# Kernel tuning notes

Measured on AMD Instinct MI355X. Metric: run time of the kernel, lower is better.

Reference implementation:

```python
import jax, jax.numpy as jnp
import numpy as np
import math

B, C, L_MIX, L_REF = 4, 512, 2048, 2048
NUM_HEADS = 8
HEAD_DIM = C // NUM_HEADS
MAX_LEN = 5000
EPS = 1e-5


def layer_norm(x, gamma, beta):
    mu = jnp.mean(x, axis=-1, keepdims=True)
    var = jnp.mean(jnp.square(x - mu), axis=-1, keepdims=True)
    return (x - mu) * jax.lax.rsqrt(var + EPS) * gamma + beta


def setup_inputs() -> dict:
    key = jax.random.key(0)
    ks = jax.random.split(key, 12)
    inp = {
        "query": jax.random.normal(ks[0], (B, C, L_MIX), dtype=jnp.float32),
        "key_value": jax.random.normal(ks[1], (B, C, L_REF), dtype=jnp.float32),
        "pos_encoding": jax.random.normal(ks[2], (1, MAX_LEN, C), dtype=jnp.float32) * 0.01,
        "q_gamma": jnp.ones((C,), jnp.float32),
        "q_beta": jnp.zeros((C,), jnp.float32),
        "k_gamma": jnp.ones((C,), jnp.float32),
        "k_beta": jnp.zeros((C,), jnp.float32),
        "Wq": jax.random.normal(ks[3], (C, C), jnp.float32) / math.sqrt(C),
        "bq": jax.random.normal(ks[4], (C,), jnp.float32) * 0.01,
        "Wk": jax.random.normal(ks[5], (C, C), jnp.float32) / math.sqrt(C),
        "bk": jax.random.normal(ks[6], (C,), jnp.float32) * 0.01,
        "Wv": jax.random.normal(ks[7], (C, C), jnp.float32) / math.sqrt(C),
        "bv": jax.random.normal(ks[8], (C,), jnp.float32) * 0.01,
        "Wo": jax.random.normal(ks[9], (C, C), jnp.float32) / math.sqrt(C),
        "bo": jax.random.normal(ks[10], (C,), jnp.float32) * 0.01,
    }
    return inp


def reference(query, key_value, pos_encoding, q_gamma, q_beta, k_gamma, k_beta,
              Wq, bq, Wk, bk, Wv, bv, Wo, bo):
    # (B, C, L) -> (B, L, C)
    q = jnp.transpose(query, (0, 2, 1))
    kv = jnp.transpose(key_value, (0, 2, 1))
    Lm, Lr = q.shape[1], kv.shape[1]
    q = q + pos_encoding[:, :Lm, :]
    kv = kv + pos_encoding[:, :Lr, :]
    q = layer_norm(q, q_gamma, q_beta)
    kv = layer_norm(kv, k_gamma, k_beta)
    Q = q @ Wq + bq          # (B, Lm, C)
    K = kv @ Wk + bk         # (B, Lr, C)
    V = kv @ Wv + bv         # (B, Lr, C)
    Q = Q.reshape(B, Lm, NUM_HEADS, HEAD_DIM)
    K = K.reshape(B, Lr, NUM_HEADS, HEAD_DIM)
    V = V.reshape(B, Lr, NUM_HEADS, HEAD_DIM)
    scale = math.sqrt(HEAD_DIM)
    scores = jnp.einsum('bqhd,bkhd->bhqk', Q, K) / scale  # (B, H, Lm, Lr)
    scores = jnp.clip(scores, -50.0, 50.0)
    attn = jax.nn.softmax(scores, axis=-1)  # dropout is identity at eval
    out = jnp.einsum('bhqk,bkhd->bqhd', attn, V).reshape(B, Lm, C)
    out = out @ Wo + bo
    out = out + q            # residual with normed/pos-encoded query, per source
    return jnp.transpose(out, (0, 2, 1))  # (B, C, Lm)
```

## Files before the change

### kernel.cpp

```cpp
#include <hip/hip_runtime.h>
#include <hip/hip_bf16.h>

#define B_ 4
#define C_ 512
#define L_ 2048
#define H_ 8
#define D_ 64
#define EPS_ 1e-5f

using short8 = __attribute__((ext_vector_type(8))) short;
using s4v    = __attribute__((ext_vector_type(4))) short;
using f32x4  = __attribute__((ext_vector_type(4))) float;

#if defined(__has_builtin)
#if __has_builtin(__builtin_amdgcn_exp2f)
#define EXP2(x) __builtin_amdgcn_exp2f(x)
#else
#define EXP2(x) exp2f(x)
#endif
#else
#define EXP2(x) exp2f(x)
#endif

#define GLOAD_LDS16(g, l)                                                     \
  __builtin_amdgcn_global_load_lds(                                           \
      (const __attribute__((address_space(1))) void*)(g),                     \
      (__attribute__((address_space(3))) void*)(l), 16, 0, 0)

static __device__ __forceinline__ short f2bf(float f) {
  __hip_bfloat16 h = __float2bfloat16(f);
  return __builtin_bit_cast(short, h);
}
static __device__ __forceinline__ float bf2f(short s) {
  return __bfloat162float(__builtin_bit_cast(__hip_bfloat16, s));
}

__global__ __launch_bounds__(256) void k_convert_w(
    const float* __restrict__ Wq, const float* __restrict__ Wk,
    const float* __restrict__ Wv, const float* __restrict__ Wo,
    short* __restrict__ Wt) {
  int m = blockIdx.x, k0 = blockIdx.y * 32, n0 = blockIdx.z * 32;
  const float* W = (m == 0) ? Wq : (m == 1) ? Wk : (m == 2) ? Wv : Wo;
  __shared__ float T[32][33];
  int t = threadIdx.x;
  {
    int kl = t >> 3, n4 = (t & 7) * 4;
    float4 v = *(const float4*)(W + (size_t)(k0 + kl) * C_ + n0 + n4);
    T[kl][n4] = v.x; T[kl][n4 + 1] = v.y; T[kl][n4 + 2] = v.z; T[kl][n4 + 3] = v.w;
  }
  __syncthreads();
  {
    int nl = t >> 3, k4 = (t & 7) * 4;
    s4v o;
#pragma unroll
    for (int j = 0; j < 4; ++j) o[j] = f2bf(T[k4 + j][nl]);
    *(s4v*)(Wt + (size_t)(m * C_ + n0 + nl) * C_ + k0 + k4) = o;
  }
}

__global__ __launch_bounds__(256) void k_prep(
    const float* __restrict__ query, const float* __restrict__ kv,
    const float* __restrict__ pos,
    const float* __restrict__ qg, const float* __restrict__ qb,
    const float* __restrict__ kg, const float* __restrict__ kb,
    short* __restrict__ qn, short* __restrict__ kvn) {
  int l0 = blockIdx.x * 16;
  int b  = blockIdx.y;
  int z  = blockIdx.z;
  const float* src = z ? kv : query;
  const float* g   = z ? kg : qg;
  const float* be  = z ? kb : qb;
  short* dst       = z ? kvn : qn;

  __shared__ alignas(16) float T[16][516];
  __shared__ float mu_s[16], rs_s[16];
  int t = threadIdx.x;

#pragma unroll
  for (int i = 0; i < 8; ++i) {
    int idx = i * 256 + t;
    int cc = idx >> 2, lg = (idx & 3) * 4;
    float4 v = *(const float4*)(src + (size_t)(b * C_ + cc) * L_ + l0 + lg);
    T[lg + 0][cc] = v.x; T[lg + 1][cc] = v.y; T[lg + 2][cc] = v.z; T[lg + 3][cc] = v.w;
  }
  __syncthreads();
#pragma unroll
  for (int i = 0; i < 8; ++i) {
    int idx = i * 256 + t;
    int ll = idx >> 7, c4 = (idx & 127) * 4;
    float4 p = *(const float4*)(pos + (size_t)(l0 + ll) * C_ + c4);
    float4* tp = (float4*)&T[ll][c4];
    float4 cur = *tp;
    cur.x += p.x; cur.y += p.y; cur.z += p.z; cur.w += p.w;
    *tp = cur;
  }
  __syncthreads();
  {
    int row = t >> 4, j = t & 15;
    float s1 = 0.f, s2 = 0.f;
    for (int c = j; c < C_; c += 16) { float v = T[row][c]; s1 += v; s2 += v * v; }
    for (int m = 1; m < 16; m <<= 1) {
      s1 += __shfl_xor(s1, m, 64);
      s2 += __shfl_xor(s2, m, 64);
    }
    if (j == 0) {
      float mu  = s1 * (1.0f / C_);
      float var = s2 * (1.0f / C_) - mu * mu;
      mu_s[row] = mu;
      rs_s[row] = rsqrtf(var + EPS_);
    }
  }
  __syncthreads();
#pragma unroll
  for (int i = 0; i < 8; ++i) {
    int idx = i * 256 + t;
    int ll = idx >> 7, c4 = (idx & 127) * 4;
    float4 v  = *(const float4*)&T[ll][c4];
    float4 gv = *(const float4*)(g + c4);
    float4 bv = *(const float4*)(be + c4);
    float mu = mu_s[ll], rs = rs_s[ll];
    s4v o;
    o[0] = f2bf((v.x - mu) * rs * gv.x + bv.x);
    o[1] = f2bf((v.y - mu) * rs * gv.y + bv.y);
    o[2] = f2bf((v.z - mu) * rs * gv.z + bv.z);
    o[3] = f2bf((v.w - mu) * rs * gv.w + bv.w);
    *(s4v*)(dst + (size_t)(b * L_ + l0 + ll) * C_ + c4) = o;
  }
}

__global__ __launch_bounds__(256) void k_gemm_qkv(
    const short* __restrict__ qn, const short* __restrict__ kvn,
    const short* __restrict__ Wt,
    const float* __restrict__ bq, const float* __restrict__ bk, const float* __restrict__ bv,
    short* __restrict__ Qw, short* __restrict__ Kw, short* __restrict__ Vtg) {
  int z = blockIdx.z;
  const short* X    = z ? kvn : qn;
  const short* W    = Wt + (size_t)z * C_ * C_;
  const float* bias = (z == 0) ? bq : (z == 1) ? bk : bv;
  float sc          = (z == 0) ? 0.18033688f : 1.0f;

  int m0 = blockIdx.x * 128, n0 = blockIdx.y * 128;
  __shared__ alignas(16) short As[128 * 32];
  __shared__ alignas(16) short Bs[128 * 32];
  int t = threadIdx.x, lane = t & 63, w = t >> 6;
  int wm = w & 1, wn = w >> 1;
  int quad = lane >> 4, c = lane & 15;

  const short* Ag = X + (size_t)(m0 + w * 32 + (lane >> 2)) * C_ + (lane & 3) * 8;
  const short* Bg = W + (size_t)(n0 + w * 32 + (lane >> 2)) * C_ + (lane & 3) * 8;

  f32x4 zero4 = {0.f, 0.f, 0.f, 0.f};
  f32x4 acc[4][4];
  for (int i = 0; i < 4; ++i) for (int j = 0; j < 4; ++j) acc[i][j] = zero4;

  for (int k0 = 0; k0 < C_; k0 += 32) {
    __syncthreads();
#pragma unroll
    for (int j = 0; j < 2; ++j) {
      GLOAD_LDS16(Ag + (size_t)j * 16 * C_ + k0, As + (w * 32 + j * 16) * 32);
      GLOAD_LDS16(Bg + (size_t)j * 16 * C_ + k0, Bs + (w * 32 + j * 16) * 32);
    }
    __syncthreads();
    short8 a[4], bf[4];
#pragma unroll
    for (int i = 0; i < 4; ++i)
      a[i]  = *(const short8*)(As + (wm * 64 + i * 16 + c) * 32 + quad * 8);
#pragma unroll
    for (int i = 0; i < 4; ++i)
      bf[i] = *(const short8*)(Bs + (wn * 64 + i * 16 + c) * 32 + quad * 8);
#pragma unroll
    for (int i = 0; i < 4; ++i)
#pragma unroll
      for (int j = 0; j < 4; ++j)
        acc[i][j] = __builtin_amdgcn_mfma_f32_16x16x32_bf16(a[i], bf[j], acc[i][j], 0, 0, 0);
  }

  if (z == 2) {
#pragma unroll
    for (int i = 0; i < 4; ++i)
#pragma unroll
      for (int j = 0; j < 4; ++j) {
        int colg = n0 + wn * 64 + j * 16 + c;
        float bia = bias[colg];
        int hh = colg >> 6, dd = colg & 63;
        int rowg = m0 + wm * 64 + i * 16 + quad * 4;
        int bb = rowg >> 11, l = rowg & (L_ - 1);
        s4v o;
#pragma unroll
        for (int r = 0; r < 4; ++r) o[r] = f2bf(acc[i][j][r] + bia);
        *(s4v*)(Vtg + ((size_t)(bb * H_ + hh) * D_ + dd) * L_ + l) = o;
      }
  } else {
    short* Y = (z == 0) ? Qw : Kw;
#pragma unroll
    for (int i = 0; i < 4; ++i)
#pragma unroll
      for (int j = 0; j < 4; ++j) {
        int colg = n0 + wn * 64 + j * 16 + c;
        float bia = bias[colg];
        int rowg = m0 + wm * 64 + i * 16 + quad * 4;
#pragma unroll
        for (int r = 0; r < 4; ++r)
          Y[(size_t)(rowg + r) * C_ + colg] = f2bf((acc[i][j][r] + bia) * sc);
      }
  }
}

#define LDP 72
#define LDC 68
__global__ __launch_bounds__(256, 2) void k_attn(
    const short* __restrict__ Qw, const short* __restrict__ Kw,
    const short* __restrict__ Vtg, short* __restrict__ Ow) {
  int bh = blockIdx.x & 31;
  int l0 = (blockIdx.x >> 5) * 128;
  int b = bh >> 3, h = bh & 7;
  __shared__ alignas(16) short Pw[4][16 * LDP];
  __shared__ alignas(16) float Cbuf[128 * LDC];
  __shared__ float Lbuf[128];
  int t = threadIdx.x, lane = t & 63, w = t >> 6;
  int qh = w & 1, ls = w >> 1;
  int quad = lane >> 4, c = lane & 15;

  short8 qa[4][2];
#pragma unroll
  for (int s = 0; s < 4; ++s) {
    const short* qp = Qw + ((size_t)(b * L_ + l0 + qh * 64 + s * 16 + c) * H_ + h) * D_ + quad * 8;
    qa[s][0] = *(const short8*)qp;
    qa[s][1] = *(const short8*)(qp + 32);
  }

  f32x4 zero4 = {0.f, 0.f, 0.f, 0.f};
  f32x4 acc[4][4];
#pragma unroll
  for (int s = 0; s < 4; ++s)
    for (int dt = 0; dt < 4; ++dt) acc[s][dt] = zero4;
  float lsum[4] = {0.f, 0.f, 0.f, 0.f};

  const short* Kb = Kw + ((size_t)(b * L_) * H_ + h) * D_;
  const short* Vb = Vtg + (size_t)(b * H_ + h) * D_ * L_;
  short* pb = &Pw[w][0];

  short8 kf[2][4][2];
  auto loadK = [&](int buf, int lr) {
#pragma unroll
    for (int T = 0; T < 4; ++T) {
      const short* kp = Kb + (size_t)(lr + T * 16 + c) * C_ + quad * 8;
      kf[buf][T][0] = *(const short8*)kp;
      kf[buf][T][1] = *(const short8*)(kp + 32);
    }
  };

  auto chunk = [&](int buf, int lr0, int lrn) {
    loadK(buf ^ 1, lrn);
    short8 vf[4][2];
#pragma unroll
    for (int dt = 0; dt < 4; ++dt) {
      const short* vp = Vb + (size_t)(dt * 16 + c) * L_ + lr0 + quad * 8;
      vf[dt][0] = *(const short8*)vp;
      vf[dt][1] = *(const short8*)(vp + 32);
    }
#pragma unroll
    for (int s = 0; s < 4; ++s) {
      f32x4 st[4] = {zero4, zero4, zero4, zero4};
#pragma unroll
      for (int T = 0; T < 4; ++T) {
        st[T] = __builtin_amdgcn_mfma_f32_16x16x32_bf16(kf[buf][T][0], qa[s][0], st[T], 0, 0, 0);
        st[T] = __builtin_amdgcn_mfma_f32_16x16x32_bf16(kf[buf][T][1], qa[s][1], st[T], 0, 0, 0);
      }
#pragma unroll
      for (int T = 0; T < 4; ++T) {
        s4v pk;
#pragma unroll
        for (int r = 0; r < 4; ++r) {
          float p = EXP2(st[T][r]);
          lsum[s] += p;
          pk[r] = f2bf(p);
        }
        *(s4v*)(pb + c * LDP + T * 16 + quad * 4) = pk;
      }
#pragma unroll
      for (int hf = 0; hf < 2; ++hf) {
        short8 pf = *(const short8*)(pb + c * LDP + hf * 32 + quad * 8);
#pragma unroll
        for (int dt = 0; dt < 4; ++dt)
          acc[s][dt] = __builtin_amdgcn_mfma_f32_16x16x32_bf16(vf[dt][hf], pf, acc[s][dt], 0, 0, 0);
      }
    }
  };

  loadK(0, ls * 64);
  for (int i = 0; i < 8; ++i) {
    int lr0 = ls * 64 + i * 256;
    chunk(0, lr0, lr0 + 128);
    chunk(1, lr0 + 128, (i == 7) ? ls * 64 : lr0 + 256);
  }

#pragma unroll
  for (int s = 0; s < 4; ++s) {
    lsum[s] += __shfl_xor(lsum[s], 16, 64);
    lsum[s] += __shfl_xor(lsum[s], 32, 64);
  }

  if (ls == 1) {
#pragma unroll
    for (int s = 0; s < 4; ++s) {
      int q = qh * 64 + s * 16 + c;
#pragma unroll
      for (int dt = 0; dt < 4; ++dt)
        *(f32x4*)(Cbuf + q * LDC + dt * 16 + quad * 4) = acc[s][dt];
      if (quad == 0) Lbuf[q] = lsum[s];
    }
  }
  __syncthreads();
  if (ls == 0) {
#pragma unroll
    for (int s = 0; s < 4; ++s) {
      int q = qh * 64 + s * 16 + c;
      float inv = 1.0f / (lsum[s] + Lbuf[q]);
#pragma unroll
      for (int dt = 0; dt < 4; ++dt) {
        f32x4 o = *(const f32x4*)(Cbuf + q * LDC + dt * 16 + quad * 4);
        s4v ov;
#pragma unroll
        for (int r = 0; r < 4; ++r) ov[r] = f2bf((acc[s][dt][r] + o[r]) * inv);
        *(s4v*)(Ow + ((size_t)(b * L_ + l0 + q) * H_ + h) * D_ + dt * 16 + quad * 4) = ov;
      }
    }
  }
}

__global__ __launch_bounds__(256) void k_gemm_out(
    const short* __restrict__ Ow, const short* __restrict__ Wot,
    const float* __restrict__ bo, const short* __restrict__ qn,
    float* __restrict__ out) {
  int m0 = blockIdx.x * 128, n0 = blockIdx.y * 128;
  __shared__ alignas(16) short As[128 * 32];
  __shared__ alignas(16) short Bs[128 * 32];
  int t = threadIdx.x, lane = t & 63, w = t >> 6;
  int wm = w & 1, wn = w >> 1;
  int quad = lane >> 4, c = lane & 15;

  const short* Ag = Ow  + (size_t)(m0 + w * 32 + (lane >> 2)) * C_ + (lane & 3) * 8;
  const short* Bg = Wot + (size_t)(n0 + w * 32 + (lane >> 2)) * C_ + (lane & 3) * 8;

  f32x4 zero4 = {0.f, 0.f, 0.f, 0.f};
  f32x4 acc[4][4];
  for (int i = 0; i < 4; ++i) for (int j = 0; j < 4; ++j) acc[i][j] = zero4;

  for (int k0 = 0; k0 < C_; k0 += 32) {
    __syncthreads();
#pragma unroll
    for (int j = 0; j < 2; ++j) {
      GLOAD_LDS16(Ag + (size_t)j * 16 * C_ + k0, As + (w * 32 + j * 16) * 32);
      GLOAD_LDS16(Bg + (size_t)j * 16 * C_ + k0, Bs + (w * 32 + j * 16) * 32);
    }
    __syncthreads();
    short8 a[4], bf[4];
#pragma unroll
    for (int i = 0; i < 4; ++i)
      a[i]  = *(const short8*)(As + (wm * 64 + i * 16 + c) * 32 + quad * 8);
#pragma unroll
    for (int i = 0; i < 4; ++i)
      bf[i] = *(const short8*)(Bs + (wn * 64 + i * 16 + c) * 32 + quad * 8);
#pragma unroll
    for (int i = 0; i < 4; ++i)
#pragma unroll
      for (int j = 0; j < 4; ++j)
        acc[i][j] = __builtin_amdgcn_mfma_f32_16x16x32_bf16(a[i], bf[j], acc[i][j], 0, 0, 0);
  }

  int bb = m0 >> 11;
#pragma unroll
  for (int i = 0; i < 4; ++i)
#pragma unroll
    for (int j = 0; j < 4; ++j) {
      int colg = n0 + wn * 64 + j * 16 + c;
      float bia = bo[colg];
      int rowg = m0 + wm * 64 + i * 16 + quad * 4;
      int l = rowg & (L_ - 1);
      float4 vv;
      float* pv = &vv.x;
#pragma unroll
      for (int r = 0; r < 4; ++r)
        pv[r] = acc[i][j][r] + bia + bf2f(qn[(size_t)(rowg + r) * C_ + colg]);
      *(float4*)(out + ((size_t)bb * C_ + colg) * L_ + l) = vv;
    }
}

extern "C" void kernel_launch(void* const* d_in, const int* in_sizes, int n_in,
                              void* d_out, int out_size, void* d_ws, size_t ws_size,
                              hipStream_t stream) {
  const float* query     = (const float*)d_in[0];
  const float* key_value = (const float*)d_in[1];
  const float* pos       = (const float*)d_in[2];
  const float* qg        = (const float*)d_in[3];
  const float* qb        = (const float*)d_in[4];
  const float* kg        = (const float*)d_in[5];
  const float* kb        = (const float*)d_in[6];
  const float* Wq        = (const float*)d_in[7];
  const float* bq        = (const float*)d_in[8];
  const float* Wk        = (const float*)d_in[9];
  const float* bk        = (const float*)d_in[10];
  const float* Wv        = (const float*)d_in[11];
  const float* bv        = (const float*)d_in[12];
  const float* Wo        = (const float*)d_in[13];
  const float* bo        = (const float*)d_in[14];
  float* out = (float*)d_out;

  char* ws = (char*)d_ws;
  const size_t SZ = (size_t)B_ * L_ * C_ * 2;
  short* qn  = (short*)(ws + 0 * SZ);
  short* kvn = (short*)(ws + 1 * SZ);
  short* Qw  = (short*)(ws + 2 * SZ);
  short* Kw  = (short*)(ws + 3 * SZ);
  short* Vtg = (short*)(ws + 4 * SZ);
  short* Ow  = (short*)(ws + 5 * SZ);
  short* Wt  = (short*)(ws + 6 * SZ);

  k_convert_w<<<dim3(4, 16, 16), 256, 0, stream>>>(Wq, Wk, Wv, Wo, Wt);
  k_prep<<<dim3(L_ / 16, B_, 2), 256, 0, stream>>>(query, key_value, pos, qg, qb, kg, kb, qn, kvn);
  k_gemm_qkv<<<dim3(8192 / 128, C_ / 128, 3), 256, 0, stream>>>(qn, kvn, Wt, bq, bk, bv, Qw, Kw, Vtg);
  k_attn<<<dim3(512), 256, 0, stream>>>(Qw, Kw, Vtg, Ow);
  k_gemm_out<<<dim3(8192 / 128, C_ / 128, 1), 256, 0, stream>>>(Ow, Wt + (size_t)3 * C_ * C_, bo, qn, out);
}
```

Baseline: 280.1 us.

## Merge weight-convert and prep kernels, widen GEMM K-tile, simplify attention loop

Fuses the weight transpose/convert kernel and the layernorm prep kernel into one launch, with block-index dispatch over a shared LDS buffer. This removes one kernel launch. Both projection GEMMs now stage 64-wide K tiles instead of 32, which halves the number of barrier pairs per tile at the cost of double the LDS. The attention loop drops the register double-buffered K prefetch in favour of a simpler per-chunk load of K and V. That lowers register pressure but exposes load latency.

```diff
diff --git a/kernel.cpp b/kernel.cpp
--- a/kernel.cpp
+++ b/kernel.cpp
@@ -35,46 +35,52 @@
   return __bfloat162float(__builtin_bit_cast(__hip_bfloat16, s));
 }
 
-__global__ __launch_bounds__(256) void k_convert_w(
+__global__ __launch_bounds__(256) void k_pre(
     const float* __restrict__ Wq, const float* __restrict__ Wk,
     const float* __restrict__ Wv, const float* __restrict__ Wo,
-    short* __restrict__ Wt) {
-  int m = blockIdx.x, k0 = blockIdx.y * 32, n0 = blockIdx.z * 32;
-  const float* W = (m == 0) ? Wq : (m == 1) ? Wk : (m == 2) ? Wv : Wo;
-  __shared__ float T[32][33];
-  int t = threadIdx.x;
-  {
-    int kl = t >> 3, n4 = (t & 7) * 4;
-    float4 v = *(const float4*)(W + (size_t)(k0 + kl) * C_ + n0 + n4);
-    T[kl][n4] = v.x; T[kl][n4 + 1] = v.y; T[kl][n4 + 2] = v.z; T[kl][n4 + 3] = v.w;
-  }
-  __syncthreads();
-  {
-    int nl = t >> 3, k4 = (t & 7) * 4;
-    s4v o;
-#pragma unroll
-    for (int j = 0; j < 4; ++j) o[j] = f2bf(T[k4 + j][nl]);
-    *(s4v*)(Wt + (size_t)(m * C_ + n0 + nl) * C_ + k0 + k4) = o;
-  }
-}
-
-__global__ __launch_bounds__(256) void k_prep(
+    short* __restrict__ Wt,
     const float* __restrict__ query, const float* __restrict__ kv,
     const float* __restrict__ pos,
     const float* __restrict__ qg, const float* __restrict__ qb,
     const float* __restrict__ kg, const float* __restrict__ kb,
     short* __restrict__ qn, short* __restrict__ kvn) {
-  int l0 = blockIdx.x * 16;
-  int b  = blockIdx.y;
-  int z  = blockIdx.z;
+  __shared__ alignas(16) float SB[16 * 516 + 32];
+  int t = threadIdx.x;
+  int id = blockIdx.x;
+
+  if (id < 1024) {
+    int m = id >> 8, rest = id & 255;
+    int k0 = (rest >> 4) * 32, n0 = (rest & 15) * 32;
+    const float* W = (m == 0) ? Wq : (m == 1) ? Wk : (m == 2) ? Wv : Wo;
+    float (*T)[33] = (float(*)[33])SB;
+    {
+      int kl = t >> 3, n4 = (t & 7) * 4;
+      float4 v = *(const float4*)(W + (size_t)(k0 + kl) * C_ + n0 + n4);
+      T[kl][n4] = v.x; T[kl][n4 + 1] = v.y; T[kl][n4 + 2] = v.z; T[kl][n4 + 3] = v.w;
+    }
+    __syncthreads();
+    {
+      int nl = t >> 3, k4 = (t & 7) * 4;
+      s4v o;
+#pragma unroll
+      for (int j = 0; j < 4; ++j) o[j] = f2bf(T[k4 + j][nl]);
+      *(s4v*)(Wt + (size_t)(m * C_ + n0 + nl) * C_ + k0 + k4) = o;
+    }
+    return;
+  }
+
+  id -= 1024;
+  int z  = id >> 9;
+  int b  = (id >> 7) & 3;
+  int l0 = (id & 127) * 16;
   const float* src = z ? kv : query;
   const float* g   = z ? kg : qg;
   const float* be  = z ? kb : qb;
   short* dst       = z ? kvn : qn;
 
-  __shared__ alignas(16) float T[16][516];
-  __shared__ float mu_s[16], rs_s[16];
-  int t = threadIdx.x;
+  float (*T)[516] = (float(*)[516])SB;
+  float* mu_s = SB + 16 * 516;
+  float* rs_s = mu_s + 16;
 
 #pragma unroll
   for (int i = 0; i < 8; ++i) {
@@ -140,39 +146,42 @@
   float sc          = (z == 0) ? 0.18033688f : 1.0f;
 
   int m0 = blockIdx.x * 128, n0 = blockIdx.y * 128;
-  __shared__ alignas(16) short As[128 * 32];
-  __shared__ alignas(16) short Bs[128 * 32];
+  __shared__ alignas(16) short As[128 * 64];
+  __shared__ alignas(16) short Bs[128 * 64];
   int t = threadIdx.x, lane = t & 63, w = t >> 6;
   int wm = w & 1, wn = w >> 1;
   int quad = lane >> 4, c = lane & 15;
 
-  const short* Ag = X + (size_t)(m0 + w * 32 + (lane >> 2)) * C_ + (lane & 3) * 8;
-  const short* Bg = W + (size_t)(n0 + w * 32 + (lane >> 2)) * C_ + (lane & 3) * 8;
+  const short* Ag = X + (size_t)(m0 + w * 32 + (lane >> 3)) * C_ + (lane & 7) * 8;
+  const short* Bg = W + (size_t)(n0 + w * 32 + (lane >> 3)) * C_ + (lane & 7) * 8;
 
   f32x4 zero4 = {0.f, 0.f, 0.f, 0.f};
   f32x4 acc[4][4];
   for (int i = 0; i < 4; ++i) for (int j = 0; j < 4; ++j) acc[i][j] = zero4;
 
-  for (int k0 = 0; k0 < C_; k0 += 32) {
+  for (int k0 = 0; k0 < C_; k0 += 64) {
     __syncthreads();
 #pragma unroll
-    for (int j = 0; j < 2; ++j) {
-      GLOAD_LDS16(Ag + (size_t)j * 16 * C_ + k0, As + (w * 32 + j * 16) * 32);
-      GLOAD_LDS16(Bg + (size_t)j * 16 * C_ + k0, Bs + (w * 32 + j * 16) * 32);
+    for (int j = 0; j < 4; ++j) {
+      GLOAD_LDS16(Ag + (size_t)(j * 8) * C_ + k0, As + (w * 32 + j * 8) * 64);
+      GLOAD_LDS16(Bg + (size_t)(j * 8) * C_ + k0, Bs + (w * 32 + j * 8) * 64);
     }
     __syncthreads();
-    short8 a[4], bf[4];
-#pragma unroll
-    for (int i = 0; i < 4; ++i)
-      a[i]  = *(const short8*)(As + (wm * 64 + i * 16 + c) * 32 + quad * 8);
-#pragma unroll
-    for (int i = 0; i < 4; ++i)
-      bf[i] = *(const short8*)(Bs + (wn * 64 + i * 16 + c) * 32 + quad * 8);
-#pragma unroll
-    for (int i = 0; i < 4; ++i)
+#pragma unroll
+    for (int kc = 0; kc < 2; ++kc) {
+      short8 a[4], bf[4];
+#pragma unroll
+      for (int i = 0; i < 4; ++i)
+        a[i]  = *(const short8*)(As + (wm * 64 + i * 16 + c) * 64 + kc * 32 + quad * 8);
 #pragma unroll
       for (int j = 0; j < 4; ++j)
-        acc[i][j] = __builtin_amdgcn_mfma_f32_16x16x32_bf16(a[i], bf[j], acc[i][j], 0, 0, 0);
+        bf[j] = *(const short8*)(Bs + (wn * 64 + j * 16 + c) * 64 + kc * 32 + quad * 8);
+#pragma unroll
+      for (int i = 0; i < 4; ++i)
+#pragma unroll
+        for (int j = 0; j < 4; ++j)
+          acc[i][j] = __builtin_amdgcn_mfma_f32_16x16x32_bf16(a[i], bf[j], acc[i][j], 0, 0, 0);
+    }
   }
 
   if (z == 2) {
@@ -240,32 +249,28 @@
   const short* Vb = Vtg + (size_t)(b * H_ + h) * D_ * L_;
   short* pb = &Pw[w][0];
 
-  short8 kf[2][4][2];
-  auto loadK = [&](int buf, int lr) {
+  for (int lr0 = ls * 64; lr0 < L_; lr0 += 128) {
+    short8 kf[4][2], vf[4][2];
 #pragma unroll
     for (int T = 0; T < 4; ++T) {
-      const short* kp = Kb + (size_t)(lr + T * 16 + c) * C_ + quad * 8;
-      kf[buf][T][0] = *(const short8*)kp;
-      kf[buf][T][1] = *(const short8*)(kp + 32);
-    }
-  };
-
-  auto chunk = [&](int buf, int lr0, int lrn) {
-    loadK(buf ^ 1, lrn);
-    short8 vf[4][2];
+      const short* kp = Kb + (size_t)(lr0 + T * 16 + c) * C_ + quad * 8;
+      kf[T][0] = *(const short8*)kp;
+      kf[T][1] = *(const short8*)(kp + 32);
+    }
 #pragma unroll
     for (int dt = 0; dt < 4; ++dt) {
       const short* vp = Vb + (size_t)(dt * 16 + c) * L_ + lr0 + quad * 8;
       vf[dt][0] = *(const short8*)vp;
       vf[dt][1] = *(const short8*)(vp + 32);
     }
+
 #pragma unroll
     for (int s = 0; s < 4; ++s) {
       f32x4 st[4] = {zero4, zero4, zero4, zero4};
 #pragma unroll
       for (int T = 0; T < 4; ++T) {
-        st[T] = __builtin_amdgcn_mfma_f32_16x16x32_bf16(kf[buf][T][0], qa[s][0], st[T], 0, 0, 0);
-        st[T] = __builtin_amdgcn_mfma_f32_16x16x32_bf16(kf[buf][T][1], qa[s][1], st[T], 0, 0, 0);
+        st[T] = __builtin_amdgcn_mfma_f32_16x16x32_bf16(kf[T][0], qa[s][0], st[T], 0, 0, 0);
+        st[T] = __builtin_amdgcn_mfma_f32_16x16x32_bf16(kf[T][1], qa[s][1], st[T], 0, 0, 0);
       }
 #pragma unroll
       for (int T = 0; T < 4; ++T) {
@@ -286,13 +291,6 @@
           acc[s][dt] = __builtin_amdgcn_mfma_f32_16x16x32_bf16(vf[dt][hf], pf, acc[s][dt], 0, 0, 0);
       }
     }
-  };
-
-  loadK(0, ls * 64);
-  for (int i = 0; i < 8; ++i) {
-    int lr0 = ls * 64 + i * 256;
-    chunk(0, lr0, lr0 + 128);
-    chunk(1, lr0 + 128, (i == 7) ? ls * 64 : lr0 + 256);
   }
 
 #pragma unroll
@@ -334,39 +332,42 @@
     const float* __restrict__ bo, const short* __restrict__ qn,
     float* __restrict__ out) {
   int m0 = blockIdx.x * 128, n0 = blockIdx.y * 128;
-  __shared__ alignas(16) short As[128 * 32];
-  __shared__ alignas(16) short Bs[128 * 32];
+  __shared__ alignas(16) short As[128 * 64];
+  __shared__ alignas(16) short Bs[128 * 64];
   int t = threadIdx.x, lane = t & 63, w = t >> 6;
   int wm = w & 1, wn = w >> 1;
   int quad = lane >> 4, c = lane & 15;
 
-  const short* Ag = Ow  + (size_t)(m0 + w * 32 + (lane >> 2)) * C_ + (lane & 3) * 8;
-  const short* Bg = Wot + (size_t)(n0 + w * 32 + (lane >> 2)) * C_ + (lane & 3) * 8;
+  const short* Ag = Ow  + (size_t)(m0 + w * 32 + (lane >> 3)) * C_ + (lane & 7) * 8;
+  const short* Bg = Wot + (size_t)(n0 + w * 32 + (lane >> 3)) * C_ + (lane & 7) * 8;
 
   f32x4 zero4 = {0.f, 0.f, 0.f, 0.f};
   f32x4 acc[4][4];
   for (int i = 0; i < 4; ++i) for (int j = 0; j < 4; ++j) acc[i][j] = zero4;
 
-  for (int k0 = 0; k0 < C_; k0 += 32) {
+  for (int k0 = 0; k0 < C_; k0 += 64) {
     __syncthreads();
 #pragma unroll
-    for (int j = 0; j < 2; ++j) {
-      GLOAD_LDS16(Ag + (size_t)j * 16 * C_ + k0, As + (w * 32 + j * 16) * 32);
-      GLOAD_LDS16(Bg + (size_t)j * 16 * C_ + k0, Bs + (w * 32 + j * 16) * 32);
+    for (int j = 0; j < 4; ++j) {
+      GLOAD_LDS16(Ag + (size_t)(j * 8) * C_ + k0, As + (w * 32 + j * 8) * 64);
+      GLOAD_LDS16(Bg + (size_t)(j * 8) * C_ + k0, Bs + (w * 32 + j * 8) * 64);
     }
     __syncthreads();
-    short8 a[4], bf[4];
-#pragma unroll
-    for (int i = 0; i < 4; ++i)
-      a[i]  = *(const short8*)(As + (wm * 64 + i * 16 + c) * 32 + quad * 8);
-#pragma unroll
-    for (int i = 0; i < 4; ++i)
-      bf[i] = *(const short8*)(Bs + (wn * 64 + i * 16 + c) * 32 + quad * 8);
-#pragma unroll
-    for (int i = 0; i < 4; ++i)
+#pragma unroll
+    for (int kc = 0; kc < 2; ++kc) {
+      short8 a[4], bf[4];
+#pragma unroll
+      for (int i = 0; i < 4; ++i)
+        a[i]  = *(const short8*)(As + (wm * 64 + i * 16 + c) * 64 + kc * 32 + quad * 8);
 #pragma unroll
       for (int j = 0; j < 4; ++j)
-        acc[i][j] = __builtin_amdgcn_mfma_f32_16x16x32_bf16(a[i], bf[j], acc[i][j], 0, 0, 0);
+        bf[j] = *(const short8*)(Bs + (wn * 64 + j * 16 + c) * 64 + kc * 32 + quad * 8);
+#pragma unroll
+      for (int i = 0; i < 4; ++i)
+#pragma unroll
+        for (int j = 0; j < 4; ++j)
+          acc[i][j] = __builtin_amdgcn_mfma_f32_16x16x32_bf16(a[i], bf[j], acc[i][j], 0, 0, 0);
+    }
   }
 
   int bb = m0 >> 11;
@@ -417,8 +418,8 @@
   short* Ow  = (short*)(ws + 5 * SZ);
   short* Wt  = (short*)(ws + 6 * SZ);
 
-  k_convert_w<<<dim3(4, 16, 16), 256, 0, stream>>>(Wq, Wk, Wv, Wo, Wt);
-  k_prep<<<dim3(L_ / 16, B_, 2), 256, 0, stream>>>(query, key_value, pos, qg, qb, kg, kb, qn, kvn);
+  k_pre<<<dim3(3072), 256, 0, stream>>>(Wq, Wk, Wv, Wo, Wt,
+                                        query, key_value, pos, qg, qb, kg, kb, qn, kvn);
   k_gemm_qkv<<<dim3(8192 / 128, C_ / 128, 3), 256, 0, stream>>>(qn, kvn, Wt, bq, bk, bv, Qw, Kw, Vtg);
   k_attn<<<dim3(512), 256, 0, stream>>>(Qw, Kw, Vtg, Ow);
   k_gemm_out<<<dim3(8192 / 128, C_ / 128, 1), 256, 0, stream>>>(Ow, Wt + (size_t)3 * C_ * C_, bo, qn, out);
```

New measurement: 235.5 us. 1.19x faster.
